# Kernel tuning notes

Measured on AMD Instinct MI355X. Metric: run time of the kernel, lower is better.

The kernel has to match this reference:

```python
import jax, jax.numpy as jnp
import numpy as np

LAMBDA_L1, LAMBDA_IOU, LAMBDA_CLS = 5.0, 2.0, 1.0
B, N, K, M = 16, 900, 91, 100


def setup_inputs() -> dict:
    key = jax.random.key(0)
    k1, k2, k3, k4, k5, k6 = jax.random.split(key, 6)
    cls_pred = jax.random.normal(k1, (B, N, K), dtype=jnp.float32)
    # valid xyxy boxes in [0,1]
    pmin = jax.random.uniform(k2, (B, N, 2), dtype=jnp.float32) * 0.5
    pwh = jax.random.uniform(k3, (B, N, 2), dtype=jnp.float32) * 0.5 + 1e-3
    bb_pred = jnp.concatenate([pmin, pmin + pwh], axis=-1)
    gmin = jax.random.uniform(k4, (B, M, 2), dtype=jnp.float32) * 0.5
    gwh = jax.random.uniform(k5, (B, M, 2), dtype=jnp.float32) * 0.5 + 1e-3
    bb_gt = jnp.concatenate([gmin, gmin + gwh], axis=-1)
    cls_gt = jax.random.randint(k6, (B, M), 0, K)
    return {"cls_pred": cls_pred, "bb_pred": bb_pred, "cls_gt": cls_gt, "bb_gt": bb_gt}


def _box_iou(b1, b2):
    # b1 [P,4], b2 [Q,4] -> iou [P,Q]
    area1 = (b1[:, 2] - b1[:, 0]) * (b1[:, 3] - b1[:, 1])
    area2 = (b2[:, 2] - b2[:, 0]) * (b2[:, 3] - b2[:, 1])
    x_min = jnp.maximum(b1[:, None, 0], b2[None, :, 0])
    y_min = jnp.maximum(b1[:, None, 1], b2[None, :, 1])
    x_max = jnp.minimum(b1[:, None, 2], b2[None, :, 2])
    y_max = jnp.minimum(b1[:, None, 3], b2[None, :, 3])
    inter = jnp.clip(x_max - x_min, 0) * jnp.clip(y_max - y_min, 0)
    union = area1[:, None] + area2[None, :] - inter
    return inter / (union + 1e-6)


def _solve(cost):
    # Jonker-Volgenant shortest augmenting path; cost (n, m) with n <= m; minimization.
    n, m = cost.shape
    u = np.zeros(n + 1)
    v = np.zeros(m + 1)
    p = np.zeros(m + 1, dtype=np.int64)   # p[j] = row matched to col j (1-indexed)
    way = np.zeros(m + 1, dtype=np.int64)
    for i in range(1, n + 1):
        p[0] = i
        j0 = 0
        minv = np.full(m + 1, np.inf)
        used = np.zeros(m + 1, dtype=bool)
        while True:
            used[j0] = True
            i0 = p[j0]
            cur = cost[i0 - 1] - u[i0] - v[1:]
            cur = np.where(used[1:], np.inf, cur)
            upd = cur < minv[1:]
            minv[1:] = np.where(upd, cur, minv[1:])
            way[1:] = np.where(upd, j0, way[1:])
            cand = np.where(used[1:], np.inf, minv[1:])
            j1 = int(np.argmin(cand)) + 1
            delta = cand[j1 - 1]
            uj = np.nonzero(used)[0]
            u[p[uj]] += delta
            v[uj] -= delta
            minv[1:] = np.where(used[1:], minv[1:], minv[1:] - delta)
            j0 = j1
            if p[j0] == 0:
                break
        while j0 != 0:
            j1 = way[j0]
            p[j0] = p[j1]
            j0 = j1
    cols = np.nonzero(p[1:])[0]
    rows = p[1:][cols] - 1
    return rows, cols


def _linear_sum_assignment(cost):
    cost = np.asarray(cost, dtype=np.float64)
    transposed = cost.shape[0] > cost.shape[1]
    rows, cols = _solve(cost.T if transposed else cost)
    if transposed:
        rows, cols = cols, rows
    order = np.argsort(rows)
    return rows[order], cols[order]


def reference(cls_pred, bb_pred, cls_gt, bb_gt):
    b, n, k = cls_pred.shape
    m = cls_gt.shape[1]
    out_prob = jax.nn.softmax(cls_pred.reshape(b * n, k), axis=-1)
    out_bbox = bb_pred.reshape(b * n, 4)
    tgt_ids = cls_gt.reshape(-1)
    tgt_bbox = bb_gt.reshape(-1, 4)
    cost_class = -out_prob[:, tgt_ids]                                   # [B*N, B*M]
    l1 = jnp.sum(jnp.abs(out_bbox[:, None, :] - tgt_bbox[None, :, :]), -1)  # p=1 cdist
    iou = -_box_iou(out_bbox, tgt_bbox)
    C = LAMBDA_IOU * iou + LAMBDA_L1 * l1 + LAMBDA_CLS * cost_class
    C = np.asarray(C.reshape(b, n, b, m))
    Cb = C[np.arange(b), :, np.arange(b), :]  # diagonal blocks [B, N, M] (= torch split(sizes)[i][i])
    preds, tgts = [], []
    for bi in range(b):
        r, c = _linear_sum_assignment(Cb[bi])
        preds.append(r)
        tgts.append(c)
    return (jnp.asarray(np.stack(preds), dtype=jnp.int64),
            jnp.asarray(np.stack(tgts), dtype=jnp.int64))
```

## Files before the change

kernel.cpp:

```cpp
#include <hip/hip_runtime.h>
#include <math.h>

#define NB 16
#define NP 900
#define NC 91
#define NT 100
#define SLOTS 15

__global__ __launch_bounds__(256) void softmax_stats_kernel(
    const float* __restrict__ cls_pred,
    float2* __restrict__ stats,
    unsigned* __restrict__ colOwner)
{
    const int b    = blockIdx.x;
    const int wid  = threadIdx.x >> 6;
    const int lane = threadIdx.x & 63;
    const int n    = blockIdx.y * 4 + wid;
    const int idx  = b * NP + n;

    if (lane == 0) colOwner[idx] = 0xFFFFFFFFu;

    const float* crow = cls_pred + (size_t)idx * NC;
    const float x0 = crow[lane];
    const float x1 = (lane + 64 < NC) ? crow[lane + 64] : -INFINITY;
    float mx = fmaxf(x0, x1);
    #pragma unroll
    for (int off = 32; off >= 1; off >>= 1)
        mx = fmaxf(mx, __shfl_xor(mx, off, 64));

    float s = expf(x0 - mx);
    if (lane + 64 < NC) s += expf(x1 - mx);
    #pragma unroll
    for (int off = 32; off >= 1; off >>= 1)
        s += __shfl_xor(s, off, 64);

    if (lane == 0) stats[idx] = make_float2(mx, 1.0f / s);
}

__global__ __launch_bounds__(256) void costrow_kernel(
    const float* __restrict__ cls_pred,
    const float* __restrict__ bb_pred,
    const int*   __restrict__ cls_gt,
    const float* __restrict__ bb_gt,
    const float2* __restrict__ stats,
    float* __restrict__ Ct,
    float* __restrict__ u_init,
    int*   __restrict__ amin,
    unsigned* __restrict__ colOwner)
{
    const int b    = blockIdx.x;
    const int wid  = threadIdx.x >> 6;
    const int lane = threadIdx.x & 63;
    const int m    = blockIdx.y * 4 + wid;
    const int row  = b * NT + m;

    const float* cpb = cls_pred + (size_t)b*NP*NC;
    const float4 gt = *reinterpret_cast<const float4*>(bb_gt + (size_t)row*4);
    const float garea = (gt.z - gt.x) * (gt.w - gt.y);
    const int   c     = cls_gt[row];

    float* outr = Ct + (size_t)row * NP;
    float best = INFINITY; int bj = 0;

    #pragma unroll
    for (int r = 0; r < SLOTS; ++r) {
        const int n = 64*r + lane;
        if ((r < SLOTS-1) || (lane < 4)) {
            const float4 bp = *reinterpret_cast<const float4*>(bb_pred + ((size_t)b*NP + n)*4);
            const float2 st = stats[b*NP + n];
            const float  x  = cpb[(size_t)n*NC + c];

            const float l1 = fabsf(bp.x - gt.x) + fabsf(bp.y - gt.y) +
                             fabsf(bp.z - gt.z) + fabsf(bp.w - gt.w);
            const float parea = (bp.z - bp.x) * (bp.w - bp.y);
            const float xm = fmaxf(bp.x, gt.x);
            const float ym = fmaxf(bp.y, gt.y);
            const float xM = fminf(bp.z, gt.z);
            const float yM = fminf(bp.w, gt.w);
            const float inter = fmaxf(xM - xm, 0.f) * fmaxf(yM - ym, 0.f);
            const float iou = inter / (parea + garea - inter + 1e-6f);
            const float pc  = expf(x - st.x) * st.y;

            const float cost = 5.0f*l1 - 2.0f*iou - pc;
            outr[n] = cost;
            if (cost < best) { best = cost; bj = n; }
        }
    }

    float vmin = best;
    #pragma unroll
    for (int off = 32; off >= 1; off >>= 1)
        vmin = fminf(vmin, __shfl_xor(vmin, off, 64));
    const unsigned long long win = __ballot(best == vmin);
    const int bjAll = __shfl(bj, __builtin_ctzll(win), 64);
    if (lane == 0) {
        u_init[row] = vmin;
        amin[row]   = bjAll;
        atomicMin(&colOwner[(size_t)b*NP + bjAll], (unsigned)m);
    }
}

__device__ __forceinline__ int pop_row(unsigned long long& fm0, unsigned long long& fm1)
{
    if (fm0) { const int l = __builtin_ctzll(fm0); fm0 &= fm0 - 1; return l + 1;  }
    if (fm1) { const int l = __builtin_ctzll(fm1); fm1 &= fm1 - 1; return l + 65; }
    return 0;
}

__global__ __launch_bounds__(64) void jv_kernel(
    const float* __restrict__ Ct,
    const float* __restrict__ u_init,
    const int*   __restrict__ amin,
    const unsigned* __restrict__ colOwner,
    int* __restrict__ out)
{
    const int b    = blockIdx.x;
    const int lane = threadIdx.x;
    const float* Cb = Ct + (size_t)b*NT*NP;

    double v[SLOTS], minv[SLOTS];
    float  cw[SLOTS], cnext[SLOTS];
    int    way[SLOTS], p[SLOTS];

    double u0 = (double)u_init[b*NT + lane];
    double u1 = (lane < NT-64) ? (double)u_init[b*NT + 64 + lane] : 0.0;

    #pragma unroll
    for (int r = 0; r < SLOTS; ++r) {
        v[r] = 0.0; way[r] = 0;
        unsigned o = 0xFFFFFFFFu;
        if ((r < SLOTS-1) || (lane < 4)) o = colOwner[(size_t)b*NP + 64*r + lane];
        p[r] = (o == 0xFFFFFFFFu) ? 0 : (int)o + 1;
    }

    const int a0 = amin[b*NT + lane];
    const bool as0 = (colOwner[(size_t)b*NP + a0] == (unsigned)lane);
    bool as1 = true;
    if (lane < NT-64) {
        const int a1 = amin[b*NT + 64 + lane];
        as1 = (colOwner[(size_t)b*NP + a1] == (unsigned)(64 + lane));
    }
    unsigned long long fm0 = __ballot(!as0);
    unsigned long long fm1 = __ballot(!as1 && (lane < NT-64));

    int iCur = pop_row(fm0, fm1);
    if (iCur) {
        const float* cr = Cb + (size_t)(iCur-1)*NP;
        #pragma unroll
        for (int r = 0; r < SLOTS; ++r) {
            int ja = 64*r + lane; if (ja > NP-1) ja = NP-1;
            cnext[r] = cr[ja];
        }
    }

    while (iCur) {
        const int iNext = pop_row(fm0, fm1);

        unsigned usedMask = 0;
        bool it0 = false, it1 = false;
        double Dtot = 0.0;
        #pragma unroll
        for (int r = 0; r < SLOTS; ++r) { minv[r] = INFINITY; cw[r] = cnext[r]; }

        const int i = iCur;
        if (i <= 64) { if (lane == i-1)  it0 = true; }
        else         { if (lane == i-65) it1 = true; }
        double ui0 = (i <= 64) ? __shfl(u0, i-1, 64) : __shfl(u1, i-65, 64);

        if (iNext) {
            const float* cr = Cb + (size_t)(iNext-1)*NP;
            #pragma unroll
            for (int r = 0; r < SLOTS; ++r) {
                int ja = 64*r + lane; if (ja > NP-1) ja = NP-1;
                cnext[r] = cr[ja];
            }
        }

        int j0 = 0, jfinal;
        while (true) {
            double best = INFINITY;
            int    pk   = 0;
            #pragma unroll
            for (int r = 0; r < SLOTS; ++r) {
                const int jm1 = 64*r + lane;
                const bool valid = ((r < SLOTS-1) || (lane < 4)) && !((usedMask >> r) & 1u);
                const double cur = valid ? (((double)cw[r] - ui0) - v[r]) : INFINITY;
                if (cur < minv[r]) { minv[r] = cur; way[r] = j0; }
                if (minv[r] < best) { best = minv[r]; pk = (jm1 + 1) | (p[r] << 10); }
            }
            double vmin = best;
            #pragma unroll
            for (int off = 32; off >= 1; off >>= 1)
                vmin = fmin(vmin, __shfl_xor(vmin, off, 64));
            const unsigned long long win = __ballot(best == vmin);
            pk = __shfl(pk, __builtin_ctzll(win), 64);

            const double delta = vmin;
            const int    j1    = pk & 1023;
            const int    pnext = pk >> 10;
            Dtot += delta;
            #pragma unroll
            for (int r = 0; r < SLOTS; ++r) minv[r] -= delta;

            #pragma unroll
            for (int r = 0; r < SLOTS; ++r) {
                if (64*r + lane + 1 == j1) {
                    usedMask |= 1u << r;
                    minv[r] = INFINITY;
                    v[r] += Dtot;
                }
            }

            if (pnext == 0) { jfinal = j1; break; }

            ui0 = (pnext <= 64) ? __shfl(u0, pnext-1, 64) : __shfl(u1, pnext-65, 64);
            if (pnext <= 64) { if (lane == pnext-1)  { u0 -= Dtot; it0 = true; } }
            else             { if (lane == pnext-65) { u1 -= Dtot; it1 = true; } }

            {
                const float* cr = Cb + (size_t)(pnext-1)*NP;
                #pragma unroll
                for (int r = 0; r < SLOTS; ++r) {
                    int ja = 64*r + lane; if (ja > NP-1) ja = NP-1;
                    cw[r] = cr[ja];
                }
            }
            j0 = j1;
        }

        {
            int jc = jfinal;
            while (jc != 0) {
                int wsel = 0;
                #pragma unroll
                for (int r = 0; r < SLOTS; ++r)
                    if (64*r + lane + 1 == jc) wsel = way[r];
                const int jprev = __shfl(wsel, (jc-1) & 63, 64);
                int newrow;
                if (jprev == 0) newrow = i;
                else {
                    int psel = 0;
                    #pragma unroll
                    for (int r = 0; r < SLOTS; ++r)
                        if (64*r + lane + 1 == jprev) psel = p[r];
                    newrow = __shfl(psel, (jprev-1) & 63, 64);
                }
                #pragma unroll
                for (int r = 0; r < SLOTS; ++r)
                    if (64*r + lane + 1 == jc) p[r] = newrow;
                jc = jprev;
            }
        }

        #pragma unroll
        for (int r = 0; r < SLOTS; ++r)
            if ((usedMask >> r) & 1u) v[r] -= Dtot;
        if (it0) u0 += Dtot;
        if (it1) u1 += Dtot;

        iCur = iNext;
    }

    int base = 0;
    #pragma unroll
    for (int r = 0; r < SLOTS; ++r) {
        const unsigned long long mask = __ballot(p[r] != 0);
        if (p[r] != 0) {
            const int rank = base + (int)__popcll(mask & ((1ull << lane) - 1ull));
            out[b*NT + rank]         = 64*r + lane;
            out[NB*NT + b*NT + rank] = p[r] - 1;
        }
        base += (int)__popcll(mask);
    }
}

extern "C" void kernel_launch(void* const* d_in, const int* in_sizes, int n_in,
                              void* d_out, int out_size, void* d_ws, size_t ws_size,
                              hipStream_t stream)
{
    const float* cls_pred = (const float*)d_in[0];
    const float* bb_pred  = (const float*)d_in[1];
    const int*   cls_gt   = (const int*)d_in[2];
    const float* bb_gt    = (const float*)d_in[3];

    char* base = (char*)d_ws;
    const size_t ctBytes    = (size_t)NB*NT*NP*sizeof(float);
    const size_t statsBytes = (size_t)NB*NP*sizeof(float2);
    float*    Ct       = (float*)base;
    float2*   stats    = (float2*)(base + ctBytes);
    unsigned* colOwner = (unsigned*)(base + ctBytes + statsBytes);
    float*    u_init   = (float*)(base + ctBytes + statsBytes + (size_t)NB*NP*4);
    int*      aminP    = (int*)(base + ctBytes + statsBytes + (size_t)NB*NP*4 + (size_t)NB*NT*4);

    softmax_stats_kernel<<<dim3(NB, NP/4), 256, 0, stream>>>(cls_pred, stats, colOwner);
    costrow_kernel<<<dim3(NB, NT/4), 256, 0, stream>>>(
        cls_pred, bb_pred, cls_gt, bb_gt, stats, Ct, u_init, aminP, colOwner);
    jv_kernel<<<NB, 64, 0, stream>>>(Ct, u_init, aminP, colOwner, (int*)d_out);
}
```

Baseline: 48.64 us.

## Fuse softmax into column-major cost build and add fp32 fast path for JV argmin

Softmax statistics and the cost computation are merged into one kernel, with one wave per prediction. Each wave keeps its probabilities in shared memory and writes one Ct column, whose stores are strided across rows. The row-min and column-claim step moves to a separate kernel that rereads Ct. In the JV inner loop, the double-precision wave reduction is replaced by a float reduction with a tolerance ballot, falling back to double only when several lanes tie, which cuts per-iteration shuffle cost in the serial solver.

```diff
diff --git a/kernel.cpp b/kernel.cpp
--- a/kernel.cpp
+++ b/kernel.cpp
@@ -7,86 +7,90 @@
 #define NT 100
 #define SLOTS 15
 
-__global__ __launch_bounds__(256) void softmax_stats_kernel(
+__global__ __launch_bounds__(256) void colcost_kernel(
     const float* __restrict__ cls_pred,
-    float2* __restrict__ stats,
+    const float* __restrict__ bb_pred,
+    const int*   __restrict__ cls_gt,
+    const float* __restrict__ bb_gt,
+    float* __restrict__ Ct,
     unsigned* __restrict__ colOwner)
 {
     const int b    = blockIdx.x;
     const int wid  = threadIdx.x >> 6;
     const int lane = threadIdx.x & 63;
     const int n    = blockIdx.y * 4 + wid;
-    const int idx  = b * NP + n;
-
-    if (lane == 0) colOwner[idx] = 0xFFFFFFFFu;
-
-    const float* crow = cls_pred + (size_t)idx * NC;
+
+    __shared__ float probs[4][NC];
+
+    if (lane == 0) colOwner[(size_t)b*NP + n] = 0xFFFFFFFFu;
+
+    const float* crow = cls_pred + ((size_t)b*NP + n)*NC;
     const float x0 = crow[lane];
     const float x1 = (lane + 64 < NC) ? crow[lane + 64] : -INFINITY;
     float mx = fmaxf(x0, x1);
     #pragma unroll
     for (int off = 32; off >= 1; off >>= 1)
         mx = fmaxf(mx, __shfl_xor(mx, off, 64));
-
     float s = expf(x0 - mx);
     if (lane + 64 < NC) s += expf(x1 - mx);
     #pragma unroll
     for (int off = 32; off >= 1; off >>= 1)
         s += __shfl_xor(s, off, 64);
-
-    if (lane == 0) stats[idx] = make_float2(mx, 1.0f / s);
-}
-
-__global__ __launch_bounds__(256) void costrow_kernel(
-    const float* __restrict__ cls_pred,
-    const float* __restrict__ bb_pred,
-    const int*   __restrict__ cls_gt,
-    const float* __restrict__ bb_gt,
-    const float2* __restrict__ stats,
-    float* __restrict__ Ct,
-    float* __restrict__ u_init,
-    int*   __restrict__ amin,
-    unsigned* __restrict__ colOwner)
-{
-    const int b    = blockIdx.x;
-    const int wid  = threadIdx.x >> 6;
-    const int lane = threadIdx.x & 63;
-    const int m    = blockIdx.y * 4 + wid;
-    const int row  = b * NT + m;
-
-    const float* cpb = cls_pred + (size_t)b*NP*NC;
-    const float4 gt = *reinterpret_cast<const float4*>(bb_gt + (size_t)row*4);
-    const float garea = (gt.z - gt.x) * (gt.w - gt.y);
-    const int   c     = cls_gt[row];
-
-    float* outr = Ct + (size_t)row * NP;
-    float best = INFINITY; int bj = 0;
-
-    #pragma unroll
-    for (int r = 0; r < SLOTS; ++r) {
-        const int n = 64*r + lane;
-        if ((r < SLOTS-1) || (lane < 4)) {
-            const float4 bp = *reinterpret_cast<const float4*>(bb_pred + ((size_t)b*NP + n)*4);
-            const float2 st = stats[b*NP + n];
-            const float  x  = cpb[(size_t)n*NC + c];
+    const float rinv = 1.0f / s;
+
+    probs[wid][lane] = expf(x0 - mx) * rinv;
+    if (lane + 64 < NC) probs[wid][lane + 64] = expf(x1 - mx) * rinv;
+    __syncthreads();
+
+    const float4 bp = *reinterpret_cast<const float4*>(bb_pred + ((size_t)b*NP + n)*4);
+    const float parea = (bp.z - bp.x) * (bp.w - bp.y);
+
+    #pragma unroll
+    for (int h = 0; h < 2; ++h) {
+        const int m = lane + 64*h;
+        if (m < NT) {
+            const int row = b*NT + m;
+            const float4 gt = *reinterpret_cast<const float4*>(bb_gt + (size_t)row*4);
+            const float garea = (gt.z - gt.x) * (gt.w - gt.y);
+            const int   c     = cls_gt[row];
 
             const float l1 = fabsf(bp.x - gt.x) + fabsf(bp.y - gt.y) +
                              fabsf(bp.z - gt.z) + fabsf(bp.w - gt.w);
-            const float parea = (bp.z - bp.x) * (bp.w - bp.y);
             const float xm = fmaxf(bp.x, gt.x);
             const float ym = fmaxf(bp.y, gt.y);
             const float xM = fminf(bp.z, gt.z);
             const float yM = fminf(bp.w, gt.w);
             const float inter = fmaxf(xM - xm, 0.f) * fmaxf(yM - ym, 0.f);
             const float iou = inter / (parea + garea - inter + 1e-6f);
-            const float pc  = expf(x - st.x) * st.y;
-
-            const float cost = 5.0f*l1 - 2.0f*iou - pc;
-            outr[n] = cost;
-            if (cost < best) { best = cost; bj = n; }
-        }
-    }
-
+            const float pc  = probs[wid][c];
+
+            Ct[(size_t)row*NP + n] = 5.0f*l1 - 2.0f*iou - pc;
+        }
+    }
+}
+
+__global__ __launch_bounds__(256) void rowmin_claim_kernel(
+    const float* __restrict__ Ct,
+    float* __restrict__ u_init,
+    int*   __restrict__ amin,
+    unsigned* __restrict__ colOwner)
+{
+    const int b    = blockIdx.x;
+    const int wid  = threadIdx.x >> 6;
+    const int lane = threadIdx.x & 63;
+    const int m    = blockIdx.y * 4 + wid;
+    const int row  = b*NT + m;
+    const float* cr = Ct + (size_t)row * NP;
+
+    float best = INFINITY; int bj = 0;
+    #pragma unroll
+    for (int r = 0; r < SLOTS; ++r) {
+        const int j = 64*r + lane;
+        if ((r < SLOTS-1) || (lane < 4)) {
+            const float x = cr[j];
+            if (x < best) { best = x; bj = j; }
+        }
+    }
     float vmin = best;
     #pragma unroll
     for (int off = 32; off >= 1; off >>= 1)
@@ -188,16 +192,28 @@
                 if (cur < minv[r]) { minv[r] = cur; way[r] = j0; }
                 if (minv[r] < best) { best = minv[r]; pk = (jm1 + 1) | (p[r] << 10); }
             }
-            double vmin = best;
+
+            const float bf = (float)best;
+            float vm32 = bf;
             #pragma unroll
             for (int off = 32; off >= 1; off >>= 1)
-                vmin = fmin(vmin, __shfl_xor(vmin, off, 64));
-            const unsigned long long win = __ballot(best == vmin);
-            pk = __shfl(pk, __builtin_ctzll(win), 64);
-
-            const double delta = vmin;
-            const int    j1    = pk & 1023;
-            const int    pnext = pk >> 10;
+                vm32 = fminf(vm32, __shfl_xor(vm32, off, 64));
+            const unsigned long long cand = __ballot(bf <= vm32 + 1e-3f);
+            int winner;
+            if (__popcll(cand) == 1) {
+                winner = __builtin_ctzll(cand);
+            } else {
+                double vm = best;
+                #pragma unroll
+                for (int off = 32; off >= 1; off >>= 1)
+                    vm = fmin(vm, __shfl_xor(vm, off, 64));
+                winner = __builtin_ctzll(__ballot(best == vm));
+            }
+            const double delta = __shfl(best, winner, 64);
+            pk = __shfl(pk, winner, 64);
+
+            const int j1    = pk & 1023;
+            const int pnext = pk >> 10;
             Dtot += delta;
             #pragma unroll
             for (int r = 0; r < SLOTS; ++r) minv[r] -= delta;
@@ -284,16 +300,14 @@
     const float* bb_gt    = (const float*)d_in[3];
 
     char* base = (char*)d_ws;
-    const size_t ctBytes    = (size_t)NB*NT*NP*sizeof(float);
-    const size_t statsBytes = (size_t)NB*NP*sizeof(float2);
+    const size_t ctBytes = (size_t)NB*NT*NP*sizeof(float);
     float*    Ct       = (float*)base;
-    float2*   stats    = (float2*)(base + ctBytes);
-    unsigned* colOwner = (unsigned*)(base + ctBytes + statsBytes);
-    float*    u_init   = (float*)(base + ctBytes + statsBytes + (size_t)NB*NP*4);
-    int*      aminP    = (int*)(base + ctBytes + statsBytes + (size_t)NB*NP*4 + (size_t)NB*NT*4);
-
-    softmax_stats_kernel<<<dim3(NB, NP/4), 256, 0, stream>>>(cls_pred, stats, colOwner);
-    costrow_kernel<<<dim3(NB, NT/4), 256, 0, stream>>>(
-        cls_pred, bb_pred, cls_gt, bb_gt, stats, Ct, u_init, aminP, colOwner);
+    unsigned* colOwner = (unsigned*)(base + ctBytes);
+    float*    u_init   = (float*)(base + ctBytes + (size_t)NB*NP*4);
+    int*      aminP    = (int*)(base + ctBytes + (size_t)NB*NP*4 + (size_t)NB*NT*4);
+
+    colcost_kernel<<<dim3(NB, NP/4), 256, 0, stream>>>(
+        cls_pred, bb_pred, cls_gt, bb_gt, Ct, colOwner);
+    rowmin_claim_kernel<<<dim3(NB, NT/4), 256, 0, stream>>>(Ct, u_init, aminP, colOwner);
     jv_kernel<<<NB, 64, 0, stream>>>(Ct, u_init, aminP, colOwner, (int*)d_out);
 }
```

Result: no change. 48.66 us (+0.0%).
